# Performance work log

Hardware: AMD Instinct MI355X
Metric: run time of the kernel (lower is better)

Reference implementation:

```python
import jax, jax.numpy as jnp
import numpy as np

T, B, Q, H = 100, 256, 2048, 1024  # steps, students, n_questions, n_hidden
NIN = 2 * Q                         # n_input = 2 * n_questions


def setup_inputs() -> dict:
    key = jax.random.key(0)
    ks = jax.random.split(key, 8)
    s = 0.02  # init scale
    return {
        "x_idx": jax.random.randint(ks[0], (T, B), 0, NIN),          # one-hot index into 2Q
        "y_idx": jax.random.randint(ks[1], (T, B), 0, Q),             # next-question one-hot index
        "truth": (jax.random.uniform(ks[2], (T, B)) > 0.5).astype(jnp.float32),
        "Wm": jax.random.normal(ks[3], (H, H), jnp.float32) * s,
        "bm": jnp.zeros((H,), jnp.float32),
        "Wx": jax.random.normal(ks[4], (H, NIN), jnp.float32) * s,
        "bx": jnp.zeros((H,), jnp.float32),
        "Wy": jax.random.normal(ks[5], (Q, H), jnp.float32) * s,
        "by": jnp.zeros((Q,), jnp.float32),
        "W_start": jax.random.normal(ks[6], (H, 1), jnp.float32) * s,
        "b_start": jnp.zeros((H,), jnp.float32),
    }


def reference(x_idx, y_idx, truth, Wm, bm, Wx, bx, Wy, by, W_start, b_start):
    # state = start(zeros(B,1)): zeros @ W_start^T + b_start -> [B, H]
    h0 = jnp.zeros((B, 1), Wm.dtype) @ W_start.T + b_start

    # lin_x(input_x) with one-hot input_x == column-select of Wx: [T, B, H]
    xproj = Wx.T[x_idx] + bx

    def step(h, xp):
        h = jnp.tanh(h @ Wm.T + bm + xp)  # Elman cell: tanh(lin_m(h) + lin_x(x))
        return h, h

    _, hiddens = jax.lax.scan(step, h0, xproj)  # hiddens: [T, B, H]

    # pred = sum(sigmoid(lin_y(h)) * y_onehot) == sigmoid(logit at y_idx)
    Wy_sel = Wy[y_idx]                                        # [T, B, H]
    logits = jnp.einsum('tbh,tbh->tb', hiddens, Wy_sel) + by[y_idx]
    pred = jax.nn.sigmoid(logits)                             # [T, B]

    # BCELoss(reduction='none'): -(t*log(p) + (1-t)*log(1-p)); stable via log_sigmoid
    loss = -(truth * jax.nn.log_sigmoid(logits) + (1.0 - truth) * jax.nn.log_sigmoid(-logits))
    return pred, loss
```

## Files before the change

### kernel.cpp

```cpp
#include <hip/hip_runtime.h>
#include <hip/hip_bf16.h>
#include <math.h>

#define T_STEPS 100
#define B 256
#define Q 2048
#define H 1024
#define NIN 4096

typedef __attribute__((ext_vector_type(8))) short bf16x8;
typedef __attribute__((ext_vector_type(4))) short bf16x4;
typedef __attribute__((ext_vector_type(4))) float f32x4;
typedef unsigned long long u64;

#define WM_BYTES (64 * 2048)
#define HLDS_OFF WM_BYTES
#define HLDS_BYTES (16 * 1024)
#define HOUT_OFF HLDS_OFF
#define LOGIT_OFF (HLDS_OFF + 2048)
#define SMEM_BYTES (WM_BYTES + HLDS_BYTES)

#define H0_OFF 0
#define H1_OFF (512 * 1024)
#define LG_OFF (1024 * 1024)
#define BAR_OFF (LG_OFF + 102400)

#define AGENT __HIP_MEMORY_SCOPE_AGENT

__device__ inline unsigned short f2bf(float f) {
    union { float f; unsigned int u; } c; c.f = f;
    unsigned int u = c.u + 0x7fffu + ((c.u >> 16) & 1u);
    return (unsigned short)(u >> 16);
}

__device__ __forceinline__ void sg_bar(unsigned* cnt, unsigned target) {
    asm volatile("s_waitcnt vmcnt(0)" ::: "memory");
    __syncthreads();
    if (threadIdx.x == 0) {
        __hip_atomic_fetch_add(cnt, 1u, __ATOMIC_RELAXED, AGENT);
        while (__hip_atomic_load(cnt, __ATOMIC_RELAXED, AGENT) < target) {}
    }
    __syncthreads();
}

__global__ void ws_init(float* __restrict__ logits, unsigned* __restrict__ bar) {
    int idx = blockIdx.x * blockDim.x + threadIdx.x;
    if (idx < T_STEPS * B) logits[idx] = 0.f;
    if (idx < 512) bar[idx] = 0u;
}

__global__ __launch_bounds__(256, 1) void rnn_persistent(
    const int* __restrict__ x_idx, const int* __restrict__ y_idx,
    const float* __restrict__ truth,
    const float* __restrict__ Wm, const float* __restrict__ bm,
    const float* __restrict__ Wx, const float* __restrict__ bx_,
    const float* __restrict__ Wy, const float* __restrict__ by,
    const float* __restrict__ b_start,
    __hip_bfloat16* __restrict__ h0buf, __hip_bfloat16* __restrict__ h1buf,
    float* __restrict__ logits, unsigned* __restrict__ bar,
    float* __restrict__ out)
{
    extern __shared__ char lds[];

    const int tid = threadIdx.x;
    const int bid = blockIdx.x;
    const int rg = bid & 15;
    const int sg = bid >> 4;
    const int sbase = sg * 16;
    const int w  = tid >> 6;
    const int l  = tid & 63;
    const int lr = l & 15;
    const int g  = l >> 4;

    unsigned* bcnt = bar + sg * 32;

    for (int it = 0; it < 64; ++it) {
        int idx4 = it * 256 + tid;
        int row  = idx4 >> 8;
        int kq   = (idx4 & 255) << 2;
        float4 v = *reinterpret_cast<const float4*>(&Wm[(size_t)(rg * 64 + row) * H + kq]);
        bf16x4 b4;
        b4[0] = (short)f2bf(v.x); b4[1] = (short)f2bf(v.y);
        b4[2] = (short)f2bf(v.z); b4[3] = (short)f2bf(v.w);
        int byte = row * 2048 + (((kq >> 3) ^ (row & 7)) << 4) + ((kq & 7) << 1);
        *reinterpret_cast<bf16x4*>(&lds[byte]) = b4;
    }
    {
        int s = tid >> 4, c8 = tid & 15;
        union { unsigned short s4[4]; u64 u; } pk;
        #pragma unroll
        for (int e = 0; e < 4; ++e) pk.s4[e] = f2bf(b_start[rg * 64 + c8 * 4 + e]);
        __hip_atomic_store((u64*)&h0buf[(size_t)(sbase + s) * H + rg * 64 + c8 * 4],
                           pk.u, __ATOMIC_RELAXED, AGENT);
    }
    float bias_r[4];
    #pragma unroll
    for (int r = 0; r < 4; ++r) {
        int gi = rg * 64 + w * 16 + g * 4 + r;
        bias_r[r] = bm[gi] + bx_[gi];
    }

    sg_bar(bcnt, 16u);

    const int arow = w * 16 + lr;
    for (int t = 0; t < T_STEPS; ++t) {
        const __hip_bfloat16* hc = (t & 1) ? h1buf : h0buf;
        __hip_bfloat16*       hn = (t & 1) ? h0buf : h1buf;

        int xc = x_idx[t * B + sbase + lr];
        int yc = y_idx[t * B + sbase + lr];
        float wx_r[4], wy_r[4];
        #pragma unroll
        for (int r = 0; r < 4; ++r) {
            int gi = rg * 64 + w * 16 + g * 4 + r;
            wx_r[r] = Wx[(size_t)gi * NIN + xc];
            wy_r[r] = Wy[(size_t)yc * H + gi];
        }

        u64 r0[8], r1[8];
        #pragma unroll
        for (int it = 0; it < 4; ++it) {
            int q = it * 256 + tid;
            int srow = q >> 6, sl = q & 63;
            const u64* src = (const u64*)&hc[(size_t)(sbase + srow) * H + sl * 8];
            r0[2 * it]     = __hip_atomic_load(src,     __ATOMIC_RELAXED, AGENT);
            r0[2 * it + 1] = __hip_atomic_load(src + 1, __ATOMIC_RELAXED, AGENT);
        }
        #pragma unroll
        for (int it = 0; it < 4; ++it) {
            int q = it * 256 + tid;
            int srow = q >> 6, sl = q & 63;
            const u64* src = (const u64*)&hc[(size_t)(sbase + srow) * H + 512 + sl * 8];
            r1[2 * it]     = __hip_atomic_load(src,     __ATOMIC_RELAXED, AGENT);
            r1[2 * it + 1] = __hip_atomic_load(src + 1, __ATOMIC_RELAXED, AGENT);
        }

        f32x4 acc = {0.f, 0.f, 0.f, 0.f};

        #pragma unroll
        for (int it = 0; it < 4; ++it) {
            int q = it * 256 + tid;
            int srow = q >> 6, sl = q & 63;
            union { u64 u[2]; bf16x8 v; } cvt;
            cvt.u[0] = r0[2 * it]; cvt.u[1] = r0[2 * it + 1];
            *reinterpret_cast<bf16x8*>(
                &lds[HLDS_OFF + srow * 1024 + ((sl ^ (srow & 7)) << 4)]) = cvt.v;
        }
        __syncthreads();
        #pragma unroll
        for (int kk = 0; kk < 16; ++kk) {
            int aslot = kk * 4 + g;
            bf16x8 a = *reinterpret_cast<const bf16x8*>(
                &lds[arow * 2048 + ((aslot ^ (arow & 7)) << 4)]);
            bf16x8 bb = *reinterpret_cast<const bf16x8*>(
                &lds[HLDS_OFF + lr * 1024 + (((kk * 4 + g) ^ (lr & 7)) << 4)]);
            acc = __builtin_amdgcn_mfma_f32_16x16x32_bf16(a, bb, acc, 0, 0, 0);
        }
        __syncthreads();
        #pragma unroll
        for (int it = 0; it < 4; ++it) {
            int q = it * 256 + tid;
            int srow = q >> 6, sl = q & 63;
            union { u64 u[2]; bf16x8 v; } cvt;
            cvt.u[0] = r1[2 * it]; cvt.u[1] = r1[2 * it + 1];
            *reinterpret_cast<bf16x8*>(
                &lds[HLDS_OFF + srow * 1024 + ((sl ^ (srow & 7)) << 4)]) = cvt.v;
        }
        __syncthreads();
        #pragma unroll
        for (int kk = 0; kk < 16; ++kk) {
            int aslot = 64 + kk * 4 + g;
            bf16x8 a = *reinterpret_cast<const bf16x8*>(
                &lds[arow * 2048 + ((aslot ^ (arow & 7)) << 4)]);
            bf16x8 bb = *reinterpret_cast<const bf16x8*>(
                &lds[HLDS_OFF + lr * 1024 + (((kk * 4 + g) ^ (lr & 7)) << 4)]);
            acc = __builtin_amdgcn_mfma_f32_16x16x32_bf16(a, bb, acc, 0, 0, 0);
        }
        __syncthreads();

        float hv[4];
        #pragma unroll
        for (int r = 0; r < 4; ++r)
            hv[r] = tanhf(acc[r] + bias_r[r] + wx_r[r]);

        {
            int row0  = w * 16 + g * 4;
            int chunk = row0 >> 3;
            bf16x4 b4;
            b4[0] = (short)f2bf(hv[0]); b4[1] = (short)f2bf(hv[1]);
            b4[2] = (short)f2bf(hv[2]); b4[3] = (short)f2bf(hv[3]);
            int byte = HOUT_OFF + lr * 128 + ((chunk ^ (lr & 7)) << 4) + ((row0 & 7) << 1);
            *reinterpret_cast<bf16x4*>(&lds[byte]) = b4;
        }
        {
            float p = hv[0] * wy_r[0] + hv[1] * wy_r[1] + hv[2] * wy_r[2] + hv[3] * wy_r[3];
            p += __shfl_down(p, 32);
            p += __shfl_down(p, 16);
            if (l < 16)
                *reinterpret_cast<float*>(&lds[LOGIT_OFF + (w * 16 + l) * 4]) = p;
        }
        __syncthreads();
        {
            int s = tid >> 4, c8 = tid & 15;
            u64 v = *reinterpret_cast<const u64*>(
                &lds[HOUT_OFF + s * 128 + (((c8 >> 1) ^ (s & 7)) << 4) + ((c8 & 1) << 3)]);
            __hip_atomic_store((u64*)&hn[(size_t)(sbase + s) * H + rg * 64 + c8 * 4],
                               v, __ATOMIC_RELAXED, AGENT);
        }
        if (tid < 16) {
            const float* lg = reinterpret_cast<const float*>(&lds[LOGIT_OFF]);
            float ps = lg[tid] + lg[16 + tid] + lg[32 + tid] + lg[48 + tid];
            atomicAdd(&logits[t * B + sbase + tid], ps);
        }
        sg_bar(bcnt, 16u * (t + 2));
    }

    {
        int ti = tid >> 4, s = tid & 15;
        int t = rg + ti * 16;
        if (t < T_STEPS) {
            int idx = t * B + sbase + s;
            float lgv = __hip_atomic_load(&logits[idx], __ATOMIC_RELAXED, AGENT);
            int yc = y_idx[idx];
            lgv += by[yc];
            float pred = 1.f / (1.f + expf(-lgv));
            float tv = truth[idx];
            float e = log1pf(expf(-fabsf(lgv)));
            float ls_pos = fminf(lgv, 0.f) - e;
            float ls_neg = fminf(-lgv, 0.f) - e;
            out[idx] = pred;
            out[T_STEPS * B + idx] = -(tv * ls_pos + (1.f - tv) * ls_neg);
        }
    }
}

extern "C" void kernel_launch(void* const* d_in, const int* in_sizes, int n_in,
                              void* d_out, int out_size, void* d_ws, size_t ws_size,
                              hipStream_t stream) {
    const int*   x_idx   = (const int*)d_in[0];
    const int*   y_idx   = (const int*)d_in[1];
    const float* truth   = (const float*)d_in[2];
    const float* Wm      = (const float*)d_in[3];
    const float* bm      = (const float*)d_in[4];
    const float* Wx      = (const float*)d_in[5];
    const float* bx_     = (const float*)d_in[6];
    const float* Wy      = (const float*)d_in[7];
    const float* by      = (const float*)d_in[8];
    const float* b_start = (const float*)d_in[10];
    float* out = (float*)d_out;

    __hip_bfloat16* h0buf  = (__hip_bfloat16*)((char*)d_ws + H0_OFF);
    __hip_bfloat16* h1buf  = (__hip_bfloat16*)((char*)d_ws + H1_OFF);
    float*          logits = (float*)((char*)d_ws + LG_OFF);
    unsigned*       bar    = (unsigned*)((char*)d_ws + BAR_OFF);

    ws_init<<<(T_STEPS * B + 255) / 256, 256, 0, stream>>>(logits, bar);

    hipFuncSetAttribute(reinterpret_cast<const void*>(rnn_persistent),
                        hipFuncAttributeMaxDynamicSharedMemorySize, SMEM_BYTES);

    void* args[] = {
        (void*)&x_idx, (void*)&y_idx, (void*)&truth,
        (void*)&Wm, (void*)&bm, (void*)&Wx, (void*)&bx_,
        (void*)&Wy, (void*)&by, (void*)&b_start,
        (void*)&h0buf, (void*)&h1buf, (void*)&logits, (void*)&bar, (void*)&out
    };
    hipLaunchCooperativeKernel(reinterpret_cast<void*>(rnn_persistent),
                               dim3(256), dim3(256), args, SMEM_BYTES, stream);
}
```

Baseline: 492.7 us.

## Keep Wm MFMA A-fragments in registers instead of LDS

Each wave now loads its 16-row slice of Wm once, converts it to bf16 and holds it in 32 bf16x8 register fragments across all timesteps. This removes the per-step LDS reads of the weight operand and shrinks LDS to the hidden-state staging area. The launch also switches from a cooperative launch to a plain launch, which relies on all 256 blocks being co-resident for the spin barrier. The cost is 128 extra VGPRs per thread, which could cause spills or reduce occupancy.

```diff
diff --git a/kernel.cpp b/kernel.cpp
--- a/kernel.cpp
+++ b/kernel.cpp
@@ -13,12 +13,10 @@
 typedef __attribute__((ext_vector_type(4))) float f32x4;
 typedef unsigned long long u64;
 
-#define WM_BYTES (64 * 2048)
-#define HLDS_OFF WM_BYTES
-#define HLDS_BYTES (16 * 1024)
-#define HOUT_OFF HLDS_OFF
-#define LOGIT_OFF (HLDS_OFF + 2048)
-#define SMEM_BYTES (WM_BYTES + HLDS_BYTES)
+#define HLDS_OFF 0
+#define HOUT_OFF 16384
+#define LOGIT_OFF (16384 + 2048)
+#define SMEM_BYTES (LOGIT_OFF + 256)
 
 #define H0_OFF 0
 #define H1_OFF (512 * 1024)
@@ -74,16 +72,25 @@
 
     unsigned* bcnt = bar + sg * 32;
 
-    for (int it = 0; it < 64; ++it) {
-        int idx4 = it * 256 + tid;
-        int row  = idx4 >> 8;
-        int kq   = (idx4 & 255) << 2;
-        float4 v = *reinterpret_cast<const float4*>(&Wm[(size_t)(rg * 64 + row) * H + kq]);
-        bf16x4 b4;
-        b4[0] = (short)f2bf(v.x); b4[1] = (short)f2bf(v.y);
-        b4[2] = (short)f2bf(v.z); b4[3] = (short)f2bf(v.w);
-        int byte = row * 2048 + (((kq >> 3) ^ (row & 7)) << 4) + ((kq & 7) << 1);
-        *reinterpret_cast<bf16x4*>(&lds[byte]) = b4;
+    bf16x8 a_frag[32];
+    {
+        const int row = rg * 64 + w * 16 + lr;
+        const float* wrow = &Wm[(size_t)row * H];
+        #pragma unroll
+        for (int half = 0; half < 2; ++half) {
+            #pragma unroll
+            for (int kk = 0; kk < 16; ++kk) {
+                int k0 = (half * 64 + kk * 4 + g) * 8;
+                float4 v0 = *reinterpret_cast<const float4*>(&wrow[k0]);
+                float4 v1 = *reinterpret_cast<const float4*>(&wrow[k0 + 4]);
+                bf16x8 f;
+                f[0] = (short)f2bf(v0.x); f[1] = (short)f2bf(v0.y);
+                f[2] = (short)f2bf(v0.z); f[3] = (short)f2bf(v0.w);
+                f[4] = (short)f2bf(v1.x); f[5] = (short)f2bf(v1.y);
+                f[6] = (short)f2bf(v1.z); f[7] = (short)f2bf(v1.w);
+                a_frag[half * 16 + kk] = f;
+            }
+        }
     }
     {
         int s = tid >> 4, c8 = tid & 15;
@@ -102,7 +109,6 @@
 
     sg_bar(bcnt, 16u);
 
-    const int arow = w * 16 + lr;
     for (int t = 0; t < T_STEPS; ++t) {
         const __hip_bfloat16* hc = (t & 1) ? h1buf : h0buf;
         __hip_bfloat16*       hn = (t & 1) ? h0buf : h1buf;
@@ -149,12 +155,9 @@
         __syncthreads();
         #pragma unroll
         for (int kk = 0; kk < 16; ++kk) {
-            int aslot = kk * 4 + g;
-            bf16x8 a = *reinterpret_cast<const bf16x8*>(
-                &lds[arow * 2048 + ((aslot ^ (arow & 7)) << 4)]);
             bf16x8 bb = *reinterpret_cast<const bf16x8*>(
                 &lds[HLDS_OFF + lr * 1024 + (((kk * 4 + g) ^ (lr & 7)) << 4)]);
-            acc = __builtin_amdgcn_mfma_f32_16x16x32_bf16(a, bb, acc, 0, 0, 0);
+            acc = __builtin_amdgcn_mfma_f32_16x16x32_bf16(a_frag[kk], bb, acc, 0, 0, 0);
         }
         __syncthreads();
         #pragma unroll
@@ -169,12 +172,9 @@
         __syncthreads();
         #pragma unroll
         for (int kk = 0; kk < 16; ++kk) {
-            int aslot = 64 + kk * 4 + g;
-            bf16x8 a = *reinterpret_cast<const bf16x8*>(
-                &lds[arow * 2048 + ((aslot ^ (arow & 7)) << 4)]);
             bf16x8 bb = *reinterpret_cast<const bf16x8*>(
                 &lds[HLDS_OFF + lr * 1024 + (((kk * 4 + g) ^ (lr & 7)) << 4)]);
-            acc = __builtin_amdgcn_mfma_f32_16x16x32_bf16(a, bb, acc, 0, 0, 0);
+            acc = __builtin_amdgcn_mfma_f32_16x16x32_bf16(a_frag[16 + kk], bb, acc, 0, 0, 0);
         }
         __syncthreads();
 
@@ -212,6 +212,7 @@
             float ps = lg[tid] + lg[16 + tid] + lg[32 + tid] + lg[48 + tid];
             atomicAdd(&logits[t * B + sbase + tid], ps);
         }
+
         sg_bar(bcnt, 16u * (t + 2));
     }
 
@@ -256,15 +257,7 @@
 
     ws_init<<<(T_STEPS * B + 255) / 256, 256, 0, stream>>>(logits, bar);
 
-    hipFuncSetAttribute(reinterpret_cast<const void*>(rnn_persistent),
-                        hipFuncAttributeMaxDynamicSharedMemorySize, SMEM_BYTES);
-
-    void* args[] = {
-        (void*)&x_idx, (void*)&y_idx, (void*)&truth,
-        (void*)&Wm, (void*)&bm, (void*)&Wx, (void*)&bx_,
-        (void*)&Wy, (void*)&by, (void*)&b_start,
-        (void*)&h0buf, (void*)&h1buf, (void*)&logits, (void*)&bar, (void*)&out
-    };
-    hipLaunchCooperativeKernel(reinterpret_cast<void*>(rnn_persistent),
-                               dim3(256), dim3(256), args, SMEM_BYTES, stream);
-}
+    rnn_persistent<<<dim3(256), dim3(256), SMEM_BYTES, stream>>>(
+        x_idx, y_idx, truth, Wm, bm, Wx, bx_, Wy, by, b_start,
+        h0buf, h1buf, logits, bar, out);
+}
```

Result: faster. 466.5 us (-5.3%).
